# Kernel optimization log

Hardware: AMD Instinct MI355X
Metric: run time of the kernel (lower is better)

The kernel has to match this reference:

```python
import jax, jax.numpy as jnp
import numpy as np

D = 1024   # embd_dim
H = 4      # number of SelectiveAttentionModule heads (each full-dim)
B, S = 4, 2048


def _layernorm(x, g, b, eps=1e-5):
    mu = jnp.mean(x, axis=-1, keepdims=True)
    var = jnp.var(x, axis=-1, keepdims=True)
    return (x - mu) * jax.lax.rsqrt(var + eps) * g + b


def setup_inputs() -> dict:
    key = jax.random.key(0)
    ks = jax.random.split(key, 16)
    sd = 1.0 / np.sqrt(D)
    x = jax.random.normal(ks[0], (B, S, D), dtype=jnp.float32)
    # per-head Q/K/V projections, stacked over head dim H ([H, in, out] layout)
    Wq = jax.random.uniform(ks[1], (H, D, D), jnp.float32, -sd, sd)
    bq = jax.random.uniform(ks[2], (H, D), jnp.float32, -sd, sd)
    Wk = jax.random.uniform(ks[3], (H, D, D), jnp.float32, -sd, sd)
    bk = jax.random.uniform(ks[4], (H, D), jnp.float32, -sd, sd)
    Wv = jax.random.uniform(ks[5], (H, D, D), jnp.float32, -sd, sd)
    bv = jax.random.uniform(ks[6], (H, D), jnp.float32, -sd, sd)
    sd1 = 1.0 / np.sqrt(H * D)
    W1 = jax.random.uniform(ks[7], (H * D, D), jnp.float32, -sd1, sd1)  # [in, out]
    b1 = jax.random.uniform(ks[8], (D,), jnp.float32, -sd1, sd1)
    W2 = jax.random.uniform(ks[9], (D, D), jnp.float32, -sd, sd)
    b2 = jax.random.uniform(ks[10], (D,), jnp.float32, -sd, sd)
    g1 = jnp.ones((D,), jnp.float32)
    be1 = jnp.zeros((D,), jnp.float32)
    g2 = jnp.ones((D,), jnp.float32)
    be2 = jnp.zeros((D,), jnp.float32)
    return {"embedding_matrix": x, "Wq": Wq, "bq": bq, "Wk": Wk, "bk": bk,
            "Wv": Wv, "bv": bv, "W1": W1, "b1": b1, "g1": g1, "be1": be1,
            "W2": W2, "b2": b2, "g2": g2, "be2": be2}


def reference(embedding_matrix, Wq, bq, Wk, bk, Wv, bv, W1, b1, g1, be1, W2, b2, g2, be2):
    x = embedding_matrix  # [B, S, D]
    # batched per-head projections: [H, B, S, D]
    q = jnp.einsum('bsd,hde->hbse', x, Wq) + bq[:, None, None, :]
    k = jnp.einsum('bsd,hde->hbse', x, Wk) + bk[:, None, None, :]
    v = jnp.einsum('bsd,hde->hbse', x, Wv) + bv[:, None, None, :]
    scale = 1.0 / jnp.sqrt(jnp.asarray(D, x.dtype))
    scores = jnp.einsum('hbse,hbte->hbst', q, k) * scale  # [H, B, S, S]
    attn = jax.nn.softmax(scores, axis=-1)
    heads = jnp.einsum('hbst,hbte->hbse', attn, v)        # [H, B, S, D]
    # torch.cat([V1..V4], dim=-1) == heads reordered to [B, S, H*D]
    concat = jnp.moveaxis(heads, 0, 2).reshape(x.shape[0], x.shape[1], H * D)
    proj = concat @ W1 + b1                               # [B, S, D]
    y = _layernorm(x + proj, g1, be1)
    return _layernorm(y + (y @ W2 + b2), g2, be2)
```

## Files before the change

### kernel.cpp

```cpp
#include <hip/hip_runtime.h>

using u16 = unsigned short;
using u32 = unsigned int;
typedef __attribute__((ext_vector_type(8))) short s16x8;
typedef __attribute__((ext_vector_type(4))) float f32x4;

typedef uint4   __attribute__((may_alias)) uint4a;
typedef ushort4 __attribute__((may_alias)) ushort4a;
typedef float4  __attribute__((may_alias)) float4a;
typedef u16     __attribute__((may_alias)) u16a;
typedef s16x8   __attribute__((may_alias)) s16x8a;

#define D_ 1024
#define H_ 4
#define B_ 4
#define S_ 2048
#define M_ 8192

#define BM 128
#define BN 128
#define BK 32

__device__ __forceinline__ float bf2f(u16 u) { return __uint_as_float(((u32)u) << 16); }
__device__ __forceinline__ u16 f2bf(float f) {
  u32 b = __float_as_uint(f);
  return (u16)((b + 0x7fffu + ((b >> 16) & 1u)) >> 16);
}

__device__ __forceinline__ void gload_lds16(const u16* g, u16* l) {
  __builtin_amdgcn_global_load_lds(
      (const __attribute__((address_space(1))) void*)g,
      (__attribute__((address_space(3))) void*)l, 16, 0, 0);
}

#define FENCE asm volatile("" ::: "memory")
#define BAR do { FENCE; __builtin_amdgcn_s_barrier(); FENCE; } while (0)
#define VMC4 asm volatile("s_waitcnt vmcnt(4)" ::: "memory")
#define VMC0 asm volatile("s_waitcnt vmcnt(0)" ::: "memory")
#define LGKM0 do { asm volatile("s_waitcnt lgkmcnt(0)" ::: "memory"); \
                   __builtin_amdgcn_sched_barrier(0); } while (0)

__device__ __forceinline__ void swz_decomp(int& x, int& y, int& z) {
  const int gx = gridDim.x, gy = gridDim.y;
  const int nwg = gx * gy * gridDim.z;
  const int flat = (blockIdx.z * gy + blockIdx.y) * gx + blockIdx.x;
  const int swz = (flat & 7) * (nwg >> 3) + (flat >> 3);
  const int t = swz >> 4, i = swz & 15;
  const int tiles_X = (gx * gridDim.z) >> 2;
  const int X = (t % tiles_X) * 4 + (i & 3);
  y = (t / tiles_X) * 4 + (i >> 2);
  z = X / gx;
  x = X % gx;
}

__global__ __launch_bounds__(256) void cvt_f32_bf16(const float* __restrict__ in,
                                                    u16* __restrict__ out, long n4) {
  long stride = (long)gridDim.x * blockDim.x;
  for (long i = (long)blockIdx.x * blockDim.x + threadIdx.x; i < n4; i += stride) {
    float4 v = ((const float4a*)in)[i];
    ushort4 o;
    o.x = f2bf(v.x); o.y = f2bf(v.y); o.z = f2bf(v.z); o.w = f2bf(v.w);
    ((ushort4a*)out)[i] = o;
  }
}

__global__ __launch_bounds__(256) void tcvt(const float* __restrict__ in,
                                            u16* __restrict__ out, int K, int N,
                                            long s_in, long s_out) {
  __shared__ float t[32][33];
  const int z = blockIdx.z;
  in += (long)z * s_in;
  out += (long)z * s_out;
  const int n0 = blockIdx.x * 32, k0 = blockIdx.y * 32;
  const int tx = threadIdx.x & 31, ty = threadIdx.x >> 5;
#pragma unroll
  for (int i = 0; i < 32; i += 8) t[ty + i][tx] = in[(long)(k0 + ty + i) * N + n0 + tx];
  __syncthreads();
#pragma unroll
  for (int i = 0; i < 32; i += 8)
    out[(long)(n0 + ty + i) * K + k0 + tx] = f2bf(t[tx][ty + i]);
}

__global__ __launch_bounds__(256) void biascat(const float* __restrict__ bq,
                                               const float* __restrict__ bk,
                                               const float* __restrict__ bv,
                                               float* __restrict__ o) {
  int i = blockIdx.x * 256 + threadIdx.x;
  float v = (i < 4096) ? bq[i] : ((i < 8192) ? bk[i - 4096] : bv[i - 8192]);
  o[i] = v;
}

__global__ __launch_bounds__(256) void dred(const float* __restrict__ dpart,
                                            float* __restrict__ drow) {
  int t = blockIdx.x * 256 + threadIdx.x;
  int z = t >> 11, row = t & 2047;
  float s = 0.f;
#pragma unroll
  for (int p = 0; p < 32; ++p) s += dpart[((long)z * 32 + p) * 2048 + row];
  drow[t] = s;
}

__device__ __forceinline__ s16x8 lds_frag(const u16* buf, int r, int jc) {
  return *(const s16x8a*)&buf[(((r << 3) + (jc ^ (r & 7)))) << 3];
}
__device__ __forceinline__ void readB(const u16* Bbuf, int wc, int lane, s16x8 (&bfr)[4][2]) {
#pragma unroll
  for (int j = 0; j < 4; ++j)
#pragma unroll
    for (int s = 0; s < 2; ++s)
      bfr[j][s] = lds_frag(Bbuf, wc * 64 + j * 16 + (lane & 15), 4 * s + (lane >> 4));
}
__device__ __forceinline__ void readA(const u16* Abuf, int q, int wr, int lane, s16x8 (&afr)[2][2]) {
#pragma unroll
  for (int il = 0; il < 2; ++il)
#pragma unroll
    for (int s = 0; s < 2; ++s)
      afr[il][s] = lds_frag(Abuf, wr * 128 + (q * 2 + il) * 16 + (lane & 15), 4 * s + (lane >> 4));
}
__device__ __forceinline__ void mfma_quad(const s16x8 (&afr)[2][2], const s16x8 (&bfr)[4][2],
                                          f32x4 (&acc)[8][4], int q) {
  __builtin_amdgcn_s_setprio(1);
#pragma unroll
  for (int s = 0; s < 2; ++s)
#pragma unroll
    for (int il = 0; il < 2; ++il)
#pragma unroll
      for (int j = 0; j < 4; ++j)
        acc[q * 2 + il][j] =
            __builtin_amdgcn_mfma_f32_16x16x32_bf16(afr[il][s], bfr[j][s], acc[q * 2 + il][j], 0, 0, 0);
  __builtin_amdgcn_s_setprio(0);
}

template <int MODE>
__device__ __forceinline__ void g256_body(
    const u16* __restrict__ A, const u16* __restrict__ Bm, u16* __restrict__ Cp,
    const float* __restrict__ bias, const float* __restrict__ bias2,
    float* __restrict__ dpart, int ldc, long sA, long sB, long sC) {
  __shared__ u16 Al[2][16384];
  __shared__ u16 Bl[2][16384];
  const int bx = blockIdx.x, by = blockIdx.y, z = blockIdx.z;
  A += (long)z * sA;
  Bm += (long)z * sB;
  const long coff = (long)z * sC;
  const int bm = by * 256, bn = bx * 256;
  const int tid = threadIdx.x;
  const int lane = tid & 63;
  const int w = tid >> 6;
  const int wr = w >> 2, wc = w & 3;
  f32x4 acc[8][4] = {};
  const int nt2 = D_ >> 7;

  auto stage = [&](const u16* src, int b0, u16* lbuf, int h, int kt) {
    const int k0 = kt << 6;
#pragma unroll
    for (int it = 0; it < 2; ++it) {
      int c = w * 128 + it * 64 + lane;
      int row = h * 128 + (c >> 3);
      int j = (c & 7) ^ (row & 7);
      gload_lds16(src + (long)(b0 + row) * D_ + (k0 + j * 8),
                  lbuf + ((h * 1024 + w * 128 + it * 64) << 3));
    }
  };

  stage(A, bm, Al[0], 0, 0);
  stage(A, bm, Al[0], 1, 0);
  stage(Bm, bn, Bl[0], 0, 0);
  stage(Bm, bn, Bl[0], 1, 0);
  stage(Bm, bn, Bl[1], 0, 1);
  stage(Bm, bn, Bl[1], 1, 1);
  VMC4;
  BAR;

  s16x8 bfr[4][2];
  for (int i2 = 0; i2 < nt2; ++i2) {
    const int t = i2 * 2;
    s16x8 afr[2][2];
    readB(Bl[0], wc, lane, bfr);
    readA(Al[0], 0, wr, lane, afr);
    stage(A, bm, Al[1], 0, t + 1);
    BAR;
    mfma_quad(afr, bfr, acc, 0);
    BAR;
    readA(Al[0], 1, wr, lane, afr);
    stage(A, bm, Al[1], 1, t + 1);
    BAR;
    mfma_quad(afr, bfr, acc, 1);
    BAR;
    readA(Al[0], 2, wr, lane, afr);
    stage(Bm, bn, Bl[0], 0, t + 2);
    BAR;
    mfma_quad(afr, bfr, acc, 2);
    BAR;
    readA(Al[0], 3, wr, lane, afr);
    stage(Bm, bn, Bl[0], 1, t + 2);
    BAR;
    mfma_quad(afr, bfr, acc, 3);
    VMC4;
    BAR;
    readB(Bl[1], wc, lane, bfr);
    readA(Al[1], 0, wr, lane, afr);
    stage(A, bm, Al[0], 0, t + 2);
    BAR;
    mfma_quad(afr, bfr, acc, 0);
    BAR;
    readA(Al[1], 1, wr, lane, afr);
    stage(A, bm, Al[0], 1, t + 2);
    BAR;
    mfma_quad(afr, bfr, acc, 1);
    BAR;
    readA(Al[1], 2, wr, lane, afr);
    stage(Bm, bn, Bl[1], 0, t + 3);
    BAR;
    mfma_quad(afr, bfr, acc, 2);
    BAR;
    readA(Al[1], 3, wr, lane, afr);
    stage(Bm, bn, Bl[1], 1, t + 3);
    BAR;
    mfma_quad(afr, bfr, acc, 3);
    VMC4;
    BAR;
  }

  if (MODE == 0) {
    const float* bb = (z == 1) ? bias2 : bias;
#pragma unroll
    for (int i = 0; i < 8; i++) {
      int mbase = bm + wr * 128 + i * 16 + ((lane >> 4) << 2);
#pragma unroll
      for (int j = 0; j < 4; j++) {
        int n = bn + wc * 64 + j * 16 + (lane & 15);
        float bv = bb[n];
#pragma unroll
        for (int r = 0; r < 4; r++)
          ((u16a*)Cp)[coff + (long)(mbase + r) * ldc + n] = f2bf(acc[i][j][r] + bv);
      }
    }
  } else {
#pragma unroll
    for (int i = 0; i < 8; i++) {
      int mbase = bm + wr * 128 + i * 16 + ((lane >> 4) << 2);
#pragma unroll
      for (int r = 0; r < 4; r++) {
        const int mm = mbase + r;
        float rowsum = 0.f;
#pragma unroll
        for (int j = 0; j < 4; j++) {
          int n = bn + wc * 64 + j * 16 + (lane & 15);
          float e = __expf(acc[i][j][r] * 0.03125f);
          ((u16a*)Cp)[coff + (long)mm * ldc + n] = f2bf(e);
          rowsum += e;
        }
        rowsum += __shfl_xor(rowsum, 1, 64);
        rowsum += __shfl_xor(rowsum, 2, 64);
        rowsum += __shfl_xor(rowsum, 4, 64);
        rowsum += __shfl_xor(rowsum, 8, 64);
        if ((lane & 15) == 0)
          dpart[((long)z * 32 + (bx * 4 + wc)) * S_ + mm] = rowsum;
      }
    }
  }
}

__global__ __launch_bounds__(512, 2) void kQK(
    const u16* __restrict__ A, const u16* __restrict__ Bm, u16* __restrict__ Cp,
    const float* __restrict__ bias, const float* __restrict__ bias2,
    float* __restrict__ dpart, int ldc, long sA, long sB, long sC) {
  g256_body<0>(A, Bm, Cp, bias, bias2, dpart, ldc, sA, sB, sC);
}
__global__ __launch_bounds__(512, 2) void kSC(
    const u16* __restrict__ A, const u16* __restrict__ Bm, u16* __restrict__ Cp,
    const float* __restrict__ bias, const float* __restrict__ bias2,
    float* __restrict__ dpart, int ldc, long sA, long sB, long sC) {
  g256_body<1>(A, Bm, Cp, bias, bias2, dpart, ldc, sA, sB, sC);
}

__device__ __forceinline__ int lds_slot(int row, int ks) {
  return row * 4 + (ks ^ ((row >> 1) & 3));
}

template <int OUT_MODE, int HAS_BIAS, int ACC>
__device__ __forceinline__ void gemm2p_body(
    const u16* __restrict__ A, const u16* __restrict__ Bm, void* __restrict__ Cp,
    const float* __restrict__ bias, float* __restrict__ drow,
    int K, int lda, int ldb, int ldc,
    long sA, long sB, long sC, long sBias, float scale) {
  __shared__ u16 Al[2][BM * BK];
  __shared__ u16 Bl[2][BN * BK];
  int bx, by, z;
  swz_decomp(bx, by, z);
  A += (long)z * sA;
  Bm += (long)z * sB;
  const long coff = (long)z * sC;
  const int bm = by * BM, bn = bx * BN;
  const int tid = threadIdx.x;
  const int lane = tid & 63;
  const int w = tid >> 6;
  const int wr = w >> 1, wc = w & 1;
  f32x4 acc[4][4] = {};

  auto stage = [&](u16* Ad, u16* Bd, int k0) {
#pragma unroll
    for (int it = 0; it < 2; ++it) {
      const int sbase = w * 128 + it * 64;
      const int slot = sbase + lane;
      const int row = slot >> 2;
      const int j = (slot & 3) ^ ((row >> 1) & 3);
      gload_lds16(A + (long)(bm + row) * lda + (k0 + j * 8), Ad + sbase * 8);
      gload_lds16(Bm + (long)(bn + row) * ldb + (k0 + j * 8), Bd + sbase * 8);
    }
  };

  stage(Al[0], Bl[0], 0);
  stage(Al[1], Bl[1], BK);
  VMC4;
  BAR;
  int cur = 0;
  for (int k0 = 0; k0 < K; k0 += BK) {
    const int ks = lane >> 4;
    s16x8 a[4], b[4];
#pragma unroll
    for (int i = 0; i < 4; i++) {
      int row = wr * 64 + i * 16 + (lane & 15);
      a[i] = *(const s16x8a*)&Al[cur][lds_slot(row, ks) * 8];
    }
#pragma unroll
    for (int j = 0; j < 4; j++) {
      int row = wc * 64 + j * 16 + (lane & 15);
      b[j] = *(const s16x8a*)&Bl[cur][lds_slot(row, ks) * 8];
    }
    LGKM0;
    BAR;
    const bool more = (k0 + 2 * BK < K);
    if (more) stage(Al[cur], Bl[cur], k0 + 2 * BK);
#pragma unroll
    for (int i = 0; i < 4; i++)
#pragma unroll
      for (int j = 0; j < 4; j++)
        acc[i][j] = __builtin_amdgcn_mfma_f32_16x16x32_bf16(a[i], b[j], acc[i][j], 0, 0, 0);
    if (more) { VMC4; } else { VMC0; }
    BAR;
    cur ^= 1;
  }

  if (OUT_MODE == 5) {
#pragma unroll
    for (int i = 0; i < 4; i++) {
      int mbase = bm + wr * 64 + i * 16 + ((lane >> 4) << 2);
      float inv[4];
#pragma unroll
      for (int r = 0; r < 4; r++) inv[r] = 1.0f / drow[(long)z * S_ + mbase + r];
#pragma unroll
      for (int j = 0; j < 4; j++) {
        int n = bn + wc * 64 + j * 16 + (lane & 15);
#pragma unroll
        for (int r = 0; r < 4; r++) {
          ((u16a*)Cp)[coff + (long)(mbase + r) * ldc + n] = f2bf(acc[i][j][r] * inv[r]);
        }
      }
    }
    return;
  }
#pragma unroll
  for (int i = 0; i < 4; i++) {
    int mbase = bm + wr * 64 + i * 16 + ((lane >> 4) << 2);
#pragma unroll
    for (int j = 0; j < 4; j++) {
      int n = bn + wc * 64 + j * 16 + (lane & 15);
      float bv = 0.f;
      if (HAS_BIAS) bv = bias[z * sBias + n];
      if (OUT_MODE == 2) {
        ushort4 o;
        o.x = f2bf(acc[i][j][0] * scale + bv);
        o.y = f2bf(acc[i][j][1] * scale + bv);
        o.z = f2bf(acc[i][j][2] * scale + bv);
        o.w = f2bf(acc[i][j][3] * scale + bv);
        long idx = coff + (long)(mbase >> 11) * ((long)D_ * S_) + (long)n * S_ + (mbase & 2047);
        *(ushort4a*)&((u16a*)Cp)[idx] = o;
      } else {
#pragma unroll
        for (int r = 0; r < 4; r++) {
          float v = acc[i][j][r] * scale + bv;
          long idx = coff + (long)(mbase + r) * ldc + n;
          if (OUT_MODE == 1) {
            ((u16a*)Cp)[idx] = f2bf(v);
          } else {
            float* Cf = (float*)Cp;
            Cf[idx] = ACC ? (Cf[idx] + v) : v;
          }
        }
      }
    }
  }
}

#define GEMM2P_ARGS \
    const u16* __restrict__ A, const u16* __restrict__ Bm, void* __restrict__ Cp, \
    const float* __restrict__ bias, float* __restrict__ drow, \
    int K, int lda, int ldb, int ldc, long sA, long sB, long sC, long sBias, float scale
#define GEMM2P_FWD A, Bm, Cp, bias, drow, K, lda, ldb, ldc, sA, sB, sC, sBias, scale

__global__ __launch_bounds__(256, 4) void kV(GEMM2P_ARGS)   { gemm2p_body<2, 1, 0>(GEMM2P_FWD); }
__global__ __launch_bounds__(256, 4) void kPV(GEMM2P_ARGS)  { gemm2p_body<5, 0, 0>(GEMM2P_FWD); }
__global__ __launch_bounds__(256, 4) void kW1a(GEMM2P_ARGS) { gemm2p_body<0, 1, 0>(GEMM2P_FWD); }
__global__ __launch_bounds__(256, 4) void kW1b(GEMM2P_ARGS) { gemm2p_body<0, 0, 1>(GEMM2P_FWD); }
__global__ __launch_bounds__(256, 4) void kW2(GEMM2P_ARGS)  { gemm2p_body<0, 1, 0>(GEMM2P_FWD); }

__global__ __launch_bounds__(256) void ln_kernel(
    const float* __restrict__ X, const float* __restrict__ R,
    const float* __restrict__ g, const float* __restrict__ be,
    float* __restrict__ Y, u16* __restrict__ Yb) {
  const long row = blockIdx.x;
  const int t = threadIdx.x, lane = t & 63, w = t >> 6;
  const long base = row * 1024 + t * 4;
  float4 a = *(const float4a*)(X + base);
  float4 b = *(const float4a*)(R + base);
  float v0 = a.x + b.x, v1 = a.y + b.y, v2 = a.z + b.z, v3 = a.w + b.w;
  float s = v0 + v1 + v2 + v3;
  float q = v0 * v0 + v1 * v1 + v2 * v2 + v3 * v3;
#pragma unroll
  for (int o = 32; o > 0; o >>= 1) { s += __shfl_xor(s, o, 64); q += __shfl_xor(q, o, 64); }
  __shared__ float rs[4], rq[4];
  if (lane == 0) { rs[w] = s; rq[w] = q; }
  __syncthreads();
  s = rs[0] + rs[1] + rs[2] + rs[3];
  q = rq[0] + rq[1] + rq[2] + rq[3];
  const float mu = s * (1.f / 1024.f);
  const float var = q * (1.f / 1024.f) - mu * mu;
  const float rstd = rsqrtf(var + 1e-5f);
  float4 gv = *(const float4a*)(g + t * 4);
  float4 bv = *(const float4a*)(be + t * 4);
  float o0 = (v0 - mu) * rstd * gv.x + bv.x;
  float o1 = (v1 - mu) * rstd * gv.y + bv.y;
  float o2 = (v2 - mu) * rstd * gv.z + bv.z;
  float o3 = (v3 - mu) * rstd * gv.w + bv.w;
  float4 o4; o4.x = o0; o4.y = o1; o4.z = o2; o4.w = o3;
  *(float4a*)(Y + base) = o4;
  if (Yb) {
    ushort4 ob; ob.x = f2bf(o0); ob.y = f2bf(o1); ob.z = f2bf(o2); ob.w = f2bf(o3);
    *(ushort4a*)(Yb + base) = ob;
  }
}

extern "C" void kernel_launch(void* const* d_in, const int* in_sizes, int n_in,
                              void* d_out, int out_size, void* d_ws, size_t ws_size,
                              hipStream_t stream) {
  const float* x   = (const float*)d_in[0];
  const float* Wq  = (const float*)d_in[1];
  const float* bq  = (const float*)d_in[2];
  const float* Wk  = (const float*)d_in[3];
  const float* bk  = (const float*)d_in[4];
  const float* Wv  = (const float*)d_in[5];
  const float* bv  = (const float*)d_in[6];
  const float* W1  = (const float*)d_in[7];
  const float* b1  = (const float*)d_in[8];
  const float* g1  = (const float*)d_in[9];
  const float* be1 = (const float*)d_in[10];
  const float* W2  = (const float*)d_in[11];
  const float* b2  = (const float*)d_in[12];
  const float* g2  = (const float*)d_in[13];
  const float* be2 = (const float*)d_in[14];
  float* out = (float*)d_out;

  const size_t NEED = 170999808ULL;
  if (ws_size < NEED) return;
  char* ws = (char*)d_ws;
  u16* xb  = (u16*)(ws + 0L);
  u16* Wqt = (u16*)(ws + 16777216L);
  u16* Wkt = (u16*)(ws + 25165824L);
  u16* Wvt = (u16*)(ws + 33554432L);
  u16* W1t = (u16*)(ws + 41943040L);
  u16* W2t = (u16*)(ws + 50331648L);
  u16* Qh  = (u16*)(ws + 52428800L);
  u16* Kh  = (u16*)(ws + 69206016L);
  u16* Vt  = (u16*)(ws + 85983232L);
  u16* Sbh = (u16*)(ws + 102760448L);
  u16* Cc2 = (u16*)(ws + 136314880L);
  float* biasQKV = (float*)(ws + 169869312L);
  float* dsum    = (float*)(ws + 169918464L);
  float* dpart   = (float*)(ws + 169951232L);
  float* proj = out;
  float* y  = (float*)Qh;
  u16*   yb = Vt;
  float* z2 = (float*)Cc2;

  dim3 blk(256);
  {
    long n4 = (long)M_ * D_ / 4;
    hipLaunchKernelGGL(cvt_f32_bf16, dim3(4096), blk, 0, stream, x, xb, n4);
  }
  hipLaunchKernelGGL(tcvt, dim3(32, 32, H_), blk, 0, stream, Wq, Wqt, D_, D_,
                     (long)D_ * D_, (long)D_ * D_);
  hipLaunchKernelGGL(tcvt, dim3(32, 32, H_), blk, 0, stream, Wk, Wkt, D_, D_,
                     (long)D_ * D_, (long)D_ * D_);
  hipLaunchKernelGGL(tcvt, dim3(32, 32, H_), blk, 0, stream, Wv, Wvt, D_, D_,
                     (long)D_ * D_, (long)D_ * D_);
  hipLaunchKernelGGL(tcvt, dim3(32, 128, 1), blk, 0, stream, W1, W1t, H_ * D_, D_, 0L, 0L);
  hipLaunchKernelGGL(tcvt, dim3(32, 32, 1), blk, 0, stream, W2, W2t, D_, D_, 0L, 0L);
  hipLaunchKernelGGL(biascat, dim3(48), blk, 0, stream, bq, bk, bv, biasQKV);

  for (int g = 0; g < 2; ++g) {
    for (int hh = 0; hh < 2; ++hh) {
      const int h = g * 2 + hh;
      const long wo = (long)h * D_ * D_;
      hipLaunchKernelGGL(kQK, dim3(4, 32, 2), dim3(512), 0, stream,
                         xb, Wqt + wo, Qh, biasQKV + (long)h * D_,
                         biasQKV + 4096 + (long)h * D_, (float*)nullptr,
                         D_, 0L, (long)H_ * D_ * D_, (long)M_ * D_);
      hipLaunchKernelGGL(kV, dim3(8, 64, 1), blk, 0, stream,
                         xb, Wvt + wo, (void*)Vt, biasQKV + 8192 + (long)h * D_,
                         (float*)nullptr, D_, D_, D_, D_, 0L, 0L, 0L, 0L, 1.0f);
      hipLaunchKernelGGL(kSC, dim3(8, 8, B_), dim3(512), 0, stream,
                         Qh, Kh, Sbh, (const float*)nullptr, (const float*)nullptr,
                         dpart, S_, (long)S_ * D_, (long)S_ * D_, (long)S_ * S_);
      hipLaunchKernelGGL(dred, dim3(32), blk, 0, stream, dpart, dsum);
      hipLaunchKernelGGL(kPV, dim3(8, 16, B_), blk, 0, stream,
                         Sbh, Vt, (void*)(Cc2 + (long)hh * D_), (const float*)nullptr, dsum,
                         S_, S_, S_, 2 * D_,
                         (long)S_ * S_, (long)D_ * S_, (long)S_ * 2 * D_, 0L, 1.0f);
    }
    if (g == 0) {
      hipLaunchKernelGGL(kW1a, dim3(8, 64, 1), blk, 0, stream,
                         Cc2, W1t + (long)g * 2 * D_, (void*)proj, b1, (float*)nullptr,
                         2 * D_, 2 * D_, H_ * D_, D_, 0L, 0L, 0L, 0L, 1.0f);
    } else {
      hipLaunchKernelGGL(kW1b, dim3(8, 64, 1), blk, 0, stream,
                         Cc2, W1t + (long)g * 2 * D_, (void*)proj, (const float*)nullptr,
                         (float*)nullptr, 2 * D_, 2 * D_, H_ * D_, D_, 0L, 0L, 0L, 0L, 1.0f);
    }
  }

  hipLaunchKernelGGL(ln_kernel, dim3(M_), blk, 0, stream, x, proj, g1, be1, y, yb);

  hipLaunchKernelGGL(kW2, dim3(8, 64, 1), blk, 0, stream,
                     yb, W2t, (void*)z2, b2, (float*)nullptr,
                     D_, D_, D_, D_, 0L, 0L, 0L, 0L, 1.0f);

  hipLaunchKernelGGL(ln_kernel, dim3(M_), blk, 0, stream, y, z2, g2, be2, out, (u16*)nullptr);
}
```

Measured before the change: 793.4 us.

## Triple-buffer gemm2p, fold row-sum reduction into PV epilogue, bf16 proj

The 128x128 GEMM body moves from a double-buffered to a triple-buffered LDS pipeline, prefetching three K-steps ahead with matching vmcnt waits so more loads stay in flight. The separate dred kernel is removed: the PV epilogue now sums the 32 softmax-denominator partials for its rows into shared memory itself. The W1 projection accumulator is stored as bf16 instead of fp32, and the first layernorm reads bf16, which cuts traffic on that intermediate. In exchange LDS use per block rises, the partial sums are recomputed by every PV column block, and the accumulated projection loses precision.

```diff
diff --git a/kernel.cpp b/kernel.cpp
--- a/kernel.cpp
+++ b/kernel.cpp
@@ -35,6 +35,7 @@
 
 #define FENCE asm volatile("" ::: "memory")
 #define BAR do { FENCE; __builtin_amdgcn_s_barrier(); FENCE; } while (0)
+#define VMC8 asm volatile("s_waitcnt vmcnt(8)" ::: "memory")
 #define VMC4 asm volatile("s_waitcnt vmcnt(4)" ::: "memory")
 #define VMC0 asm volatile("s_waitcnt vmcnt(0)" ::: "memory")
 #define LGKM0 do { asm volatile("s_waitcnt lgkmcnt(0)" ::: "memory"); \
@@ -88,16 +89,6 @@
   int i = blockIdx.x * 256 + threadIdx.x;
   float v = (i < 4096) ? bq[i] : ((i < 8192) ? bk[i - 4096] : bv[i - 8192]);
   o[i] = v;
-}
-
-__global__ __launch_bounds__(256) void dred(const float* __restrict__ dpart,
-                                            float* __restrict__ drow) {
-  int t = blockIdx.x * 256 + threadIdx.x;
-  int z = t >> 11, row = t & 2047;
-  float s = 0.f;
-#pragma unroll
-  for (int p = 0; p < 32; ++p) s += dpart[((long)z * 32 + p) * 2048 + row];
-  drow[t] = s;
 }
 
 __device__ __forceinline__ s16x8 lds_frag(const u16* buf, int r, int jc) {
@@ -278,14 +269,15 @@
   return row * 4 + (ks ^ ((row >> 1) & 3));
 }
 
-template <int OUT_MODE, int HAS_BIAS, int ACC>
+template <int OUT_MODE, int HAS_BIAS>
 __device__ __forceinline__ void gemm2p_body(
     const u16* __restrict__ A, const u16* __restrict__ Bm, void* __restrict__ Cp,
-    const float* __restrict__ bias, float* __restrict__ drow,
+    const float* __restrict__ bias, float* __restrict__ dpart,
     int K, int lda, int ldb, int ldc,
     long sA, long sB, long sC, long sBias, float scale) {
-  __shared__ u16 Al[2][BM * BK];
-  __shared__ u16 Bl[2][BN * BK];
+  __shared__ u16 Al[3][BM * BK];
+  __shared__ u16 Bl[3][BN * BK];
+  __shared__ float sinv[BM];
   int bx, by, z;
   swz_decomp(bx, by, z);
   A += (long)z * sA;
@@ -312,7 +304,8 @@
 
   stage(Al[0], Bl[0], 0);
   stage(Al[1], Bl[1], BK);
-  VMC4;
+  stage(Al[2], Bl[2], 2 * BK);
+  VMC8;
   BAR;
   int cur = 0;
   for (int k0 = 0; k0 < K; k0 += BK) {
@@ -330,31 +323,40 @@
     }
     LGKM0;
     BAR;
-    const bool more = (k0 + 2 * BK < K);
-    if (more) stage(Al[cur], Bl[cur], k0 + 2 * BK);
+    if (k0 + 3 * BK < K) stage(Al[cur], Bl[cur], k0 + 3 * BK);
 #pragma unroll
     for (int i = 0; i < 4; i++)
 #pragma unroll
       for (int j = 0; j < 4; j++)
         acc[i][j] = __builtin_amdgcn_mfma_f32_16x16x32_bf16(a[i], b[j], acc[i][j], 0, 0, 0);
-    if (more) { VMC4; } else { VMC0; }
-    BAR;
-    cur ^= 1;
+    if (k0 + 3 * BK < K) { VMC8; }
+    else if (k0 + 2 * BK < K) { VMC4; }
+    else { VMC0; }
+    BAR;
+    cur = (cur == 2) ? 0 : cur + 1;
   }
 
   if (OUT_MODE == 5) {
+    if (tid < BM) {
+      const int row = bm + tid;
+      float s = 0.f;
+#pragma unroll
+      for (int p = 0; p < 32; ++p) s += dpart[((long)z * 32 + p) * S_ + row];
+      sinv[tid] = 1.0f / s;
+    }
+    __syncthreads();
 #pragma unroll
     for (int i = 0; i < 4; i++) {
-      int mbase = bm + wr * 64 + i * 16 + ((lane >> 4) << 2);
+      int mloc = wr * 64 + i * 16 + ((lane >> 4) << 2);
       float inv[4];
 #pragma unroll
-      for (int r = 0; r < 4; r++) inv[r] = 1.0f / drow[(long)z * S_ + mbase + r];
+      for (int r = 0; r < 4; r++) inv[r] = sinv[mloc + r];
 #pragma unroll
       for (int j = 0; j < 4; j++) {
         int n = bn + wc * 64 + j * 16 + (lane & 15);
 #pragma unroll
         for (int r = 0; r < 4; r++) {
-          ((u16a*)Cp)[coff + (long)(mbase + r) * ldc + n] = f2bf(acc[i][j][r] * inv[r]);
+          ((u16a*)Cp)[coff + (long)(bm + mloc + r) * ldc + n] = f2bf(acc[i][j][r] * inv[r]);
         }
       }
     }
@@ -383,9 +385,11 @@
           long idx = coff + (long)(mbase + r) * ldc + n;
           if (OUT_MODE == 1) {
             ((u16a*)Cp)[idx] = f2bf(v);
+          } else if (OUT_MODE == 6) {
+            u16a* Cb = (u16a*)Cp;
+            Cb[idx] = f2bf(bf2f(Cb[idx]) + v);
           } else {
-            float* Cf = (float*)Cp;
-            Cf[idx] = ACC ? (Cf[idx] + v) : v;
+            ((float*)Cp)[idx] = v;
           }
         }
       }
@@ -395,26 +399,34 @@
 
 #define GEMM2P_ARGS \
     const u16* __restrict__ A, const u16* __restrict__ Bm, void* __restrict__ Cp, \
-    const float* __restrict__ bias, float* __restrict__ drow, \
+    const float* __restrict__ bias, float* __restrict__ dpart, \
     int K, int lda, int ldb, int ldc, long sA, long sB, long sC, long sBias, float scale
-#define GEMM2P_FWD A, Bm, Cp, bias, drow, K, lda, ldb, ldc, sA, sB, sC, sBias, scale
-
-__global__ __launch_bounds__(256, 4) void kV(GEMM2P_ARGS)   { gemm2p_body<2, 1, 0>(GEMM2P_FWD); }
-__global__ __launch_bounds__(256, 4) void kPV(GEMM2P_ARGS)  { gemm2p_body<5, 0, 0>(GEMM2P_FWD); }
-__global__ __launch_bounds__(256, 4) void kW1a(GEMM2P_ARGS) { gemm2p_body<0, 1, 0>(GEMM2P_FWD); }
-__global__ __launch_bounds__(256, 4) void kW1b(GEMM2P_ARGS) { gemm2p_body<0, 0, 1>(GEMM2P_FWD); }
-__global__ __launch_bounds__(256, 4) void kW2(GEMM2P_ARGS)  { gemm2p_body<0, 1, 0>(GEMM2P_FWD); }
-
+#define GEMM2P_FWD A, Bm, Cp, bias, dpart, K, lda, ldb, ldc, sA, sB, sC, sBias, scale
+
+__global__ __launch_bounds__(256, 4) void kV(GEMM2P_ARGS)   { gemm2p_body<2, 1>(GEMM2P_FWD); }
+__global__ __launch_bounds__(256, 4) void kPV(GEMM2P_ARGS)  { gemm2p_body<5, 0>(GEMM2P_FWD); }
+__global__ __launch_bounds__(256, 4) void kW1a(GEMM2P_ARGS) { gemm2p_body<1, 1>(GEMM2P_FWD); }
+__global__ __launch_bounds__(256, 4) void kW1b(GEMM2P_ARGS) { gemm2p_body<6, 0>(GEMM2P_FWD); }
+__global__ __launch_bounds__(256, 4) void kW2(GEMM2P_ARGS)  { gemm2p_body<0, 1>(GEMM2P_FWD); }
+
+template <int RBF>
 __global__ __launch_bounds__(256) void ln_kernel(
-    const float* __restrict__ X, const float* __restrict__ R,
+    const float* __restrict__ X, const void* __restrict__ R,
     const float* __restrict__ g, const float* __restrict__ be,
     float* __restrict__ Y, u16* __restrict__ Yb) {
   const long row = blockIdx.x;
   const int t = threadIdx.x, lane = t & 63, w = t >> 6;
   const long base = row * 1024 + t * 4;
   float4 a = *(const float4a*)(X + base);
-  float4 b = *(const float4a*)(R + base);
-  float v0 = a.x + b.x, v1 = a.y + b.y, v2 = a.z + b.z, v3 = a.w + b.w;
+  float r0, r1, r2, r3;
+  if (RBF) {
+    ushort4 rb = *(const ushort4a*)((const u16*)R + base);
+    r0 = bf2f(rb.x); r1 = bf2f(rb.y); r2 = bf2f(rb.z); r3 = bf2f(rb.w);
+  } else {
+    float4 b = *(const float4a*)((const float*)R + base);
+    r0 = b.x; r1 = b.y; r2 = b.z; r3 = b.w;
+  }
+  float v0 = a.x + r0, v1 = a.y + r1, v2 = a.z + r2, v3 = a.w + r3;
   float s = v0 + v1 + v2 + v3;
   float q = v0 * v0 + v1 * v1 + v2 * v2 + v3 * v3;
 #pragma unroll
@@ -476,9 +488,8 @@
   u16* Sbh = (u16*)(ws + 102760448L);
   u16* Cc2 = (u16*)(ws + 136314880L);
   float* biasQKV = (float*)(ws + 169869312L);
-  float* dsum    = (float*)(ws + 169918464L);
   float* dpart   = (float*)(ws + 169951232L);
-  float* proj = out;
+  u16* projb = (u16*)out;
   float* y  = (float*)Qh;
   u16*   yb = Vt;
   float* z2 = (float*)Cc2;
@@ -512,28 +523,29 @@
       hipLaunchKernelGGL(kSC, dim3(8, 8, B_), dim3(512), 0, stream,
                          Qh, Kh, Sbh, (const float*)nullptr, (const float*)nullptr,
                          dpart, S_, (long)S_ * D_, (long)S_ * D_, (long)S_ * S_);
-      hipLaunchKernelGGL(dred, dim3(32), blk, 0, stream, dpart, dsum);
       hipLaunchKernelGGL(kPV, dim3(8, 16, B_), blk, 0, stream,
-                         Sbh, Vt, (void*)(Cc2 + (long)hh * D_), (const float*)nullptr, dsum,
+                         Sbh, Vt, (void*)(Cc2 + (long)hh * D_), (const float*)nullptr, dpart,
                          S_, S_, S_, 2 * D_,
                          (long)S_ * S_, (long)D_ * S_, (long)S_ * 2 * D_, 0L, 1.0f);
     }
     if (g == 0) {
       hipLaunchKernelGGL(kW1a, dim3(8, 64, 1), blk, 0, stream,
-                         Cc2, W1t + (long)g * 2 * D_, (void*)proj, b1, (float*)nullptr,
+                         Cc2, W1t + (long)g * 2 * D_, (void*)projb, b1, (float*)nullptr,
                          2 * D_, 2 * D_, H_ * D_, D_, 0L, 0L, 0L, 0L, 1.0f);
     } else {
       hipLaunchKernelGGL(kW1b, dim3(8, 64, 1), blk, 0, stream,
-                         Cc2, W1t + (long)g * 2 * D_, (void*)proj, (const float*)nullptr,
+                         Cc2, W1t + (long)g * 2 * D_, (void*)projb, (const float*)nullptr,
                          (float*)nullptr, 2 * D_, 2 * D_, H_ * D_, D_, 0L, 0L, 0L, 0L, 1.0f);
     }
   }
 
-  hipLaunchKernelGGL(ln_kernel, dim3(M_), blk, 0, stream, x, proj, g1, be1, y, yb);
+  hipLaunchKernelGGL((ln_kernel<1>), dim3(M_), blk, 0, stream, x, (const void*)projb,
+                     g1, be1, y, yb);
 
   hipLaunchKernelGGL(kW2, dim3(8, 64, 1), blk, 0, stream,
                      yb, W2t, (void*)z2, b2, (float*)nullptr,
                      D_, D_, D_, D_, 0L, 0L, 0L, 0L, 1.0f);
 
-  hipLaunchKernelGGL(ln_kernel, dim3(M_), blk, 0, stream, y, z2, g2, be2, out, (u16*)nullptr);
-}
+  hipLaunchKernelGGL((ln_kernel<0>), dim3(M_), blk, 0, stream, y, (const void*)z2,
+                     g2, be2, out, (u16*)nullptr);
+}
```

Measured after the change: 782.2 us. No clear change (-1.4%).
